# Optimization experiments

Measured on AMD Instinct MI355X. Metric: run time of the kernel, lower is better.

Reference implementation:

```python
import jax, jax.numpy as jnp
import numpy as np

# ---- Cl(4,1) Cayley table (conformal GA: metric +,+,+,+,-) ----
_METRIC = (1.0, 1.0, 1.0, 1.0, -1.0)

def _reorder_sign(a, b):
    # sign from counting swaps to bring blade product to canonical order
    a >>= 1
    s = 0
    while a:
        s += bin(a & b).count("1")
        a >>= 1
    return -1.0 if (s & 1) else 1.0

def _build_cayley():
    C = np.zeros((32, 32, 32), dtype=np.float32)
    for a in range(32):
        for b in range(32):
            s = _reorder_sign(a, b)
            common = a & b
            for i in range(5):
                if (common >> i) & 1:
                    s *= _METRIC[i]
            C[a, b, a ^ b] += s
    return C

CAYLEY = _build_cayley()  # [32,32,32]; out_k = sum_ij C[i,j,k] x_i y_j

EPS = 1e-8

def normalize_cl41(x):
    n = jnp.sqrt(jnp.sum(x * x, axis=-1, keepdims=True))
    return x / (n + EPS)


def setup_inputs() -> dict:
    key = jax.random.key(0)
    k_x, k_wi, k_bi, k_wo, k_bo = jax.random.split(key, 5)
    B, S, D, H = 64, 2048, 6, 8
    x = jax.random.normal(k_x, (B, S, D), dtype=jnp.float32)
    W_in = jax.random.normal(k_wi, (D, H * 32), dtype=jnp.float32) * (1.0 / np.sqrt(D))
    b_in = jax.random.normal(k_bi, (H * 32,), dtype=jnp.float32) * 0.01
    W_out = jax.random.normal(k_wo, (H * 32, 32), dtype=jnp.float32) * (1.0 / np.sqrt(H * 32))
    b_out = jax.random.normal(k_bo, (32,), dtype=jnp.float32) * 0.01
    return {"x": x, "W_in": W_in, "b_in": b_in, "W_out": W_out, "b_out": b_out}


def reference(x, W_in, b_in, W_out, b_out):
    B, S, D = x.shape
    H = W_in.shape[1] // 32
    C = jnp.asarray(CAYLEY)
    # project inputs to per-channel multivectors: (B,S,H,32)
    u = (x @ W_in + b_in).reshape(B, S, H, 32)
    # initial rotor state: identity (scalar blade = 1)
    psi0 = jnp.zeros((B, H, 32), dtype=x.dtype).at[..., 0].set(1.0)

    def step(psi, u_t):  # u_t: (B,H,32)
        delta = normalize_cl41(u_t.at[..., 0].add(1.0))
        psi = normalize_cl41(jnp.einsum("bhi,bhj,ijk->bhk", delta, psi, C))
        return psi, psi

    _, psi_seq = jax.lax.scan(step, psi0, jnp.swapaxes(u, 0, 1))  # (S,B,H,32)
    out = normalize_cl41(psi_seq.reshape(S, B, H * 32) @ W_out + b_out)  # (S,B,32)
    return jnp.swapaxes(out, 0, 1)  # (B,S,32)
```

## Files before the change

### kernel.cpp

```cpp
#include <hip/hip_runtime.h>
#include <hip/hip_bf16.h>
#include <stdint.h>

#define BB 64
#define SS 2048
#define DD 6
#define HH 8
#define NCH 512
#define CHUNKS 256
#define LCH 8

typedef unsigned short ushort_t;
typedef __attribute__((ext_vector_type(8))) __bf16 bf16x8;
typedef __attribute__((ext_vector_type(4))) float f32x4;

struct SignTab { float s[32][32]; };

constexpr int popc5_c(unsigned v) {
    int c = 0;
    for (int i = 0; i < 5; ++i) c += (v >> i) & 1u;
    return c;
}

constexpr SignTab make_signs() {
    SignTab t{};
    for (int a = 0; a < 32; ++a) {
        for (int b = 0; b < 32; ++b) {
            int cnt = 0;
            unsigned aa = ((unsigned)a) >> 1;
            while (aa) { cnt += popc5_c(aa & (unsigned)b); aa >>= 1; }
            if ((a & b) & 16) cnt += 1;
            t.s[a][b] = (cnt & 1) ? -1.0f : 1.0f;
        }
    }
    return t;
}

constexpr SignTab SGN = make_signs();

__device__ __forceinline__ void gp_cl41(const float* __restrict__ a,
                                        const float* __restrict__ b,
                                        float* __restrict__ o) {
#pragma unroll
    for (int k = 0; k < 32; ++k) o[k] = 0.0f;
#pragma unroll
    for (int i = 0; i < 32; ++i) {
#pragma unroll
        for (int k = 0; k < 32; ++k) {
            o[k] = fmaf(SGN.s[i][i ^ k] * a[i], b[i ^ k], o[k]);
        }
    }
}

__device__ __forceinline__ float sumsq32(const float* v) {
    float n0 = 0.f, n1 = 0.f, n2 = 0.f, n3 = 0.f;
#pragma unroll
    for (int k = 0; k < 32; k += 4) {
        n0 = fmaf(v[k+0], v[k+0], n0);
        n1 = fmaf(v[k+1], v[k+1], n1);
        n2 = fmaf(v[k+2], v[k+2], n2);
        n3 = fmaf(v[k+3], v[k+3], n3);
    }
    return (n0 + n1) + (n2 + n3);
}

__device__ __forceinline__ float rsq(float n) {
    return __builtin_amdgcn_rsqf(n);
}

__device__ __forceinline__ uint32_t f2bf_rne(float f) {
    uint32_t u = __float_as_uint(f);
    return (u + 0x7FFFu + ((u >> 16) & 1u)) >> 16;
}

__device__ __forceinline__ uint32_t packh2(float a, float b) {
    union { _Float16 h[2]; uint32_t u; } t;
    t.h[0] = (_Float16)a; t.h[1] = (_Float16)b;
    return t.u;
}
__device__ __forceinline__ float h2lo(uint32_t u) {
    union { uint32_t u32; _Float16 h[2]; } t; t.u32 = u; return (float)t.h[0];
}
__device__ __forceinline__ float h2hi(uint32_t u) {
    union { uint32_t u32; _Float16 h[2]; } t; t.u32 = u; return (float)t.h[1];
}

__device__ __forceinline__ void pack_store16(ushort_t* dst, const float* v, float scale) {
    uint32_t pk[16];
#pragma unroll
    for (int m = 0; m < 16; ++m)
        pk[m] = packh2(v[2*m] * scale, v[2*m+1] * scale);
    uint4* d4 = (uint4*)dst;
#pragma unroll
    for (int m = 0; m < 4; ++m)
        d4[m] = make_uint4(pk[4*m], pk[4*m+1], pk[4*m+2], pk[4*m+3]);
}

__device__ __forceinline__ void load_unpack16(const ushort_t* src, float* v) {
    const uint4* s4 = (const uint4*)src;
#pragma unroll
    for (int m = 0; m < 4; ++m) {
        uint4 t4 = s4[m];
        uint32_t uu[4] = { t4.x, t4.y, t4.z, t4.w };
#pragma unroll
        for (int z = 0; z < 4; ++z) {
            v[8*m + 2*z]     = h2lo(uu[z]);
            v[8*m + 2*z + 1] = h2hi(uu[z]);
        }
    }
}

__global__ __launch_bounds__(256) void k_local(
        const float* __restrict__ x, const float* __restrict__ W_in,
        const float* __restrict__ b_in, ushort_t* __restrict__ psi_loc,
        float* __restrict__ Tbuf) {
    __shared__ float4 sW4[8][57];
    for (int idx = threadIdx.x; idx < 8 * 56; idx += 256) {
        int h = idx / 56, r = idx % 56;
        float4 v;
        if (r < 48) {
            int d = r / 8, j4 = r % 8;
            const float* p = W_in + d * 256 + h * 32 + 4 * j4;
            v = make_float4(p[0], p[1], p[2], p[3]);
        } else {
            const float* p = b_in + h * 32 + 4 * (r - 48);
            v = make_float4(p[0], p[1], p[2], p[3]);
        }
        sW4[h][r] = v;
    }
    __syncthreads();

    int tid = blockIdx.x * 256 + threadIdx.x;
    int c  = tid >> 9;
    int bh = tid & 511;
    int b = bh >> 3, h = bh & 7;

    float4 bias4[8];
#pragma unroll
    for (int j4 = 0; j4 < 8; ++j4) bias4[j4] = sW4[h][48 + j4];

    float p[32];
#pragma unroll
    for (int k = 0; k < 32; ++k) p[k] = 0.f;
    p[0] = 1.f;

    const float* xrow = x + ((size_t)b * SS + (size_t)c * LCH) * DD;
    ushort_t* psi_base = psi_loc + (((size_t)b * SS + (size_t)c * LCH) * HH + h) * 32;

    float xc[12];
    {
        const float4* xp = (const float4*)xrow;
#pragma unroll
        for (int m = 0; m < 3; ++m) {
            float4 t4 = xp[m];
            xc[4*m+0] = t4.x; xc[4*m+1] = t4.y; xc[4*m+2] = t4.z; xc[4*m+3] = t4.w;
        }
    }

#pragma unroll 1
    for (int pr = 0; pr < LCH / 2; ++pr) {
        float x0[6], x1[6];
#pragma unroll
        for (int d = 0; d < 6; ++d) { x0[d] = xc[d]; x1[d] = xc[6 + d]; }

        if (pr < LCH / 2 - 1) {
            const float4* xp = (const float4*)(xrow + (pr + 1) * 12);
#pragma unroll
            for (int m = 0; m < 3; ++m) {
                float4 t4 = xp[m];
                xc[4*m+0] = t4.x; xc[4*m+1] = t4.y; xc[4*m+2] = t4.z; xc[4*m+3] = t4.w;
            }
        }

        float dl0[32], dl1[32];
#pragma unroll
        for (int j4 = 0; j4 < 8; ++j4) {
            float4 bv = bias4[j4];
            dl0[4*j4+0] = bv.x; dl0[4*j4+1] = bv.y; dl0[4*j4+2] = bv.z; dl0[4*j4+3] = bv.w;
            dl1[4*j4+0] = bv.x; dl1[4*j4+1] = bv.y; dl1[4*j4+2] = bv.z; dl1[4*j4+3] = bv.w;
        }
#pragma unroll
        for (int d = 0; d < 6; ++d) {
            float a0 = x0[d], a1 = x1[d];
#pragma unroll
            for (int j4 = 0; j4 < 8; ++j4) {
                float4 w = sW4[h][d * 8 + j4];
                dl0[4*j4+0] = fmaf(a0, w.x, dl0[4*j4+0]);
                dl0[4*j4+1] = fmaf(a0, w.y, dl0[4*j4+1]);
                dl0[4*j4+2] = fmaf(a0, w.z, dl0[4*j4+2]);
                dl0[4*j4+3] = fmaf(a0, w.w, dl0[4*j4+3]);
                dl1[4*j4+0] = fmaf(a1, w.x, dl1[4*j4+0]);
                dl1[4*j4+1] = fmaf(a1, w.y, dl1[4*j4+1]);
                dl1[4*j4+2] = fmaf(a1, w.z, dl1[4*j4+2]);
                dl1[4*j4+3] = fmaf(a1, w.w, dl1[4*j4+3]);
            }
        }
        dl0[0] += 1.0f;
        dl1[0] += 1.0f;

        float o[32];
        gp_cl41(dl0, p, o);
        pack_store16(psi_base + (size_t)(2 * pr) * HH * 32, o, rsq(sumsq32(o)));
        gp_cl41(dl1, o, p);
        pack_store16(psi_base + (size_t)(2 * pr + 1) * HH * 32, p, rsq(sumsq32(p)));
    }

    float inv = rsq(sumsq32(p));
    float* dst = Tbuf + ((size_t)bh * CHUNKS + c) * 32;
#pragma unroll
    for (int k = 0; k < 32; ++k) dst[k] = p[k] * inv;
}

__global__ __launch_bounds__(128) void k_scan_totals(
        const float* __restrict__ Tbuf, float* __restrict__ Ebuf) {
    __shared__ float sT[128][33];
    int chain = blockIdx.x;
    int pp = threadIdx.x;

    float t0[32], t1[32];
    {
        const float* s0 = Tbuf + ((size_t)chain * CHUNKS + 2 * pp) * 32;
#pragma unroll
        for (int k = 0; k < 32; ++k) t0[k] = s0[k];
#pragma unroll
        for (int k = 0; k < 32; ++k) t1[k] = s0[32 + k];
    }

    float v[32];
    {
        float o[32];
        gp_cl41(t1, t0, o);
        float inv = rsq(sumsq32(o));
#pragma unroll
        for (int k = 0; k < 32; ++k) { v[k] = o[k] * inv; sT[pp][k] = v[k]; }
    }
    __syncthreads();

#pragma unroll 1
    for (int off = 1; off < 128; off <<= 1) {
        float w[32];
        bool act = (pp >= off);
        if (act) {
#pragma unroll
            for (int k = 0; k < 32; ++k) w[k] = sT[pp - off][k];
        }
        __syncthreads();
        if (act) {
            float o[32];
            gp_cl41(v, w, o);
            float inv = rsq(sumsq32(o));
#pragma unroll
            for (int k = 0; k < 32; ++k) { v[k] = o[k] * inv; sT[pp][k] = v[k]; }
        }
        __syncthreads();
    }

    float e0[32];
    if (pp == 0) {
#pragma unroll
        for (int k = 0; k < 32; ++k) e0[k] = (k == 0) ? 1.f : 0.f;
    } else {
#pragma unroll
        for (int k = 0; k < 32; ++k) e0[k] = sT[pp - 1][k];
    }
    float e1[32];
    gp_cl41(t0, e0, e1);
    float inv1 = rsq(sumsq32(e1));

    float* d0 = Ebuf + ((size_t)chain * CHUNKS + 2 * pp) * 32;
#pragma unroll
    for (int k = 0; k < 32; ++k) d0[k] = e0[k];
#pragma unroll
    for (int k = 0; k < 32; ++k) d0[32 + k] = e1[k] * inv1;
}

__global__ __launch_bounds__(256) void k_fixup_proj(
        const ushort_t* __restrict__ psi_loc, const float* __restrict__ Ebuf,
        const float* __restrict__ W_out, const float* __restrict__ b_out,
        float* __restrict__ out) {
    int lane = threadIdx.x & 63;
    int wv = threadIdx.x >> 6;
    int q = lane >> 4;
    int n0 = lane & 15;

    bf16x8 Bf[2][8];
#pragma unroll
    for (int nt = 0; nt < 2; ++nt)
#pragma unroll
        for (int kk = 0; kk < 8; ++kk) {
            union { ushort_t u[8]; bf16x8 v; } tmp;
#pragma unroll
            for (int j = 0; j < 8; ++j)
                tmp.u[j] = (ushort_t)f2bf_rne(W_out[(kk * 32 + q * 8 + j) * 32 + nt * 16 + n0]);
            Bf[nt][kk] = tmp.v;
        }
    float bn0 = b_out[n0], bn1 = b_out[16 + n0];

    __shared__ ushort_t psiT[4][16][264];

    int tile = blockIdx.x * 4 + wv;
    int rr0 = tile * 16;
    int b = rr0 >> 11;
    int s0 = rr0 & 2047;

#pragma unroll
    for (int pp = 0; pp < 2; ++pp) {
        int row_local = pp * 8 + (lane >> 3);
        int h = lane & 7;
        int s = s0 + row_local;
        int c = s >> 3;
        int bh = b * 8 + h;

        float a[32], w[32], o[32];
        load_unpack16(psi_loc + (((size_t)b * SS + s) * HH + h) * 32, a);
        const float* e = Ebuf + ((size_t)bh * CHUNKS + c) * 32;
#pragma unroll
        for (int k = 0; k < 32; ++k) w[k] = e[k];

        gp_cl41(a, w, o);
        float inv = rsq(sumsq32(o));

        uint32_t pk[16];
#pragma unroll
        for (int m = 0; m < 16; ++m)
            pk[m] = f2bf_rne(o[2*m] * inv) | (f2bf_rne(o[2*m+1] * inv) << 16);
        uint4* dst = (uint4*)&psiT[wv][row_local][h * 32];
#pragma unroll
        for (int m = 0; m < 4; ++m)
            dst[m] = make_uint4(pk[4*m], pk[4*m+1], pk[4*m+2], pk[4*m+3]);
    }

    __syncthreads();

    f32x4 acc0 = {0.f, 0.f, 0.f, 0.f};
    f32x4 acc1 = {0.f, 0.f, 0.f, 0.f};
#pragma unroll
    for (int kk = 0; kk < 8; ++kk) {
        bf16x8 af = *(const bf16x8*)&psiT[wv][n0][kk * 32 + q * 8];
        acc0 = __builtin_amdgcn_mfma_f32_16x16x32_bf16(af, Bf[0][kk], acc0, 0, 0, 0);
        acc1 = __builtin_amdgcn_mfma_f32_16x16x32_bf16(af, Bf[1][kk], acc1, 0, 0, 0);
    }

    float c0[4], c1[4], ss[4];
#pragma unroll
    for (int i = 0; i < 4; ++i) {
        c0[i] = acc0[i] + bn0;
        c1[i] = acc1[i] + bn1;
        ss[i] = c0[i] * c0[i] + c1[i] * c1[i];
    }
#pragma unroll
    for (int m = 1; m < 16; m <<= 1) {
#pragma unroll
        for (int i = 0; i < 4; ++i) ss[i] += __shfl_xor(ss[i], m);
    }
#pragma unroll
    for (int i = 0; i < 4; ++i) {
        float inv = rsq(ss[i]);
        int row = rr0 + q * 4 + i;
        out[(size_t)row * 32 + n0]      = c0[i] * inv;
        out[(size_t)row * 32 + 16 + n0] = c1[i] * inv;
    }
}

extern "C" void kernel_launch(void* const* d_in, const int* in_sizes, int n_in,
                              void* d_out, int out_size, void* d_ws, size_t ws_size,
                              hipStream_t stream) {
    const float* x     = (const float*)d_in[0];
    const float* W_in  = (const float*)d_in[1];
    const float* b_in  = (const float*)d_in[2];
    const float* W_out = (const float*)d_in[3];
    const float* b_out = (const float*)d_in[4];
    float* out = (float*)d_out;

    char* ws = (char*)d_ws;
    ushort_t* psi  = (ushort_t*)ws;
    float* Tbuf = (float*)(ws + (size_t)64 * 1024 * 1024);
    float* Ebuf = Tbuf;

    k_local      <<< 512, 256, 0, stream>>>(x, W_in, b_in, psi, Tbuf);
    k_scan_totals<<< 512, 128, 0, stream>>>(Tbuf, Ebuf);
    k_fixup_proj <<<2048, 256, 0, stream>>>(psi, Ebuf, W_out, b_out, out);
}
```

Baseline: 203.7 us.

## Recompute local rotor scan in projection kernel instead of storing per-step psi

Result: slower. 423.8 us (+108.1%).

```diff
diff --git a/kernel.cpp b/kernel.cpp
--- a/kernel.cpp
+++ b/kernel.cpp
@@ -7,8 +7,8 @@
 #define DD 6
 #define HH 8
 #define NCH 512
-#define CHUNKS 256
-#define LCH 8
+#define CHUNKS 512
+#define LCH 4
 
 typedef unsigned short ushort_t;
 typedef __attribute__((ext_vector_type(8))) __bf16 bf16x8;
@@ -73,48 +73,38 @@
     return (u + 0x7FFFu + ((u >> 16) & 1u)) >> 16;
 }
 
-__device__ __forceinline__ uint32_t packh2(float a, float b) {
-    union { _Float16 h[2]; uint32_t u; } t;
-    t.h[0] = (_Float16)a; t.h[1] = (_Float16)b;
-    return t.u;
-}
-__device__ __forceinline__ float h2lo(uint32_t u) {
-    union { uint32_t u32; _Float16 h[2]; } t; t.u32 = u; return (float)t.h[0];
-}
-__device__ __forceinline__ float h2hi(uint32_t u) {
-    union { uint32_t u32; _Float16 h[2]; } t; t.u32 = u; return (float)t.h[1];
-}
-
-__device__ __forceinline__ void pack_store16(ushort_t* dst, const float* v, float scale) {
-    uint32_t pk[16];
-#pragma unroll
-    for (int m = 0; m < 16; ++m)
-        pk[m] = packh2(v[2*m] * scale, v[2*m+1] * scale);
-    uint4* d4 = (uint4*)dst;
-#pragma unroll
-    for (int m = 0; m < 4; ++m)
-        d4[m] = make_uint4(pk[4*m], pk[4*m+1], pk[4*m+2], pk[4*m+3]);
-}
-
-__device__ __forceinline__ void load_unpack16(const ushort_t* src, float* v) {
-    const uint4* s4 = (const uint4*)src;
-#pragma unroll
-    for (int m = 0; m < 4; ++m) {
-        uint4 t4 = s4[m];
-        uint32_t uu[4] = { t4.x, t4.y, t4.z, t4.w };
-#pragma unroll
-        for (int z = 0; z < 4; ++z) {
-            v[8*m + 2*z]     = h2lo(uu[z]);
-            v[8*m + 2*z + 1] = h2hi(uu[z]);
-        }
-    }
-}
-
-__global__ __launch_bounds__(256) void k_local(
-        const float* __restrict__ x, const float* __restrict__ W_in,
-        const float* __restrict__ b_in, ushort_t* __restrict__ psi_loc,
-        float* __restrict__ Tbuf) {
-    __shared__ float4 sW4[8][57];
+__device__ __forceinline__ void delta_pair(const float4 (*sW4)[57], int h,
+                                           const float* x0, const float* x1,
+                                           float* dl0, float* dl1) {
+#pragma unroll
+    for (int j4 = 0; j4 < 8; ++j4) {
+        float4 bv = sW4[h][48 + j4];
+        dl0[4*j4+0] = bv.x; dl0[4*j4+1] = bv.y; dl0[4*j4+2] = bv.z; dl0[4*j4+3] = bv.w;
+        dl1[4*j4+0] = bv.x; dl1[4*j4+1] = bv.y; dl1[4*j4+2] = bv.z; dl1[4*j4+3] = bv.w;
+    }
+#pragma unroll
+    for (int d = 0; d < 6; ++d) {
+        float a0 = x0[d], a1 = x1[d];
+#pragma unroll
+        for (int j4 = 0; j4 < 8; ++j4) {
+            float4 w = sW4[h][d * 8 + j4];
+            dl0[4*j4+0] = fmaf(a0, w.x, dl0[4*j4+0]);
+            dl0[4*j4+1] = fmaf(a0, w.y, dl0[4*j4+1]);
+            dl0[4*j4+2] = fmaf(a0, w.z, dl0[4*j4+2]);
+            dl0[4*j4+3] = fmaf(a0, w.w, dl0[4*j4+3]);
+            dl1[4*j4+0] = fmaf(a1, w.x, dl1[4*j4+0]);
+            dl1[4*j4+1] = fmaf(a1, w.y, dl1[4*j4+1]);
+            dl1[4*j4+2] = fmaf(a1, w.z, dl1[4*j4+2]);
+            dl1[4*j4+3] = fmaf(a1, w.w, dl1[4*j4+3]);
+        }
+    }
+    dl0[0] += 1.0f;
+    dl1[0] += 1.0f;
+}
+
+__device__ __forceinline__ void stage_W(const float* __restrict__ W_in,
+                                        const float* __restrict__ b_in,
+                                        float4 (*sW4)[57]) {
     for (int idx = threadIdx.x; idx < 8 * 56; idx += 256) {
         int h = idx / 56, r = idx % 56;
         float4 v;
@@ -128,6 +118,13 @@
         }
         sW4[h][r] = v;
     }
+}
+
+__global__ __launch_bounds__(256, 3) void k_totals(
+        const float* __restrict__ x, const float* __restrict__ W_in,
+        const float* __restrict__ b_in, float* __restrict__ Tbuf) {
+    __shared__ float4 sW4[8][57];
+    stage_W(W_in, b_in, sW4);
     __syncthreads();
 
     int tid = blockIdx.x * 256 + threadIdx.x;
@@ -135,74 +132,28 @@
     int bh = tid & 511;
     int b = bh >> 3, h = bh & 7;
 
-    float4 bias4[8];
-#pragma unroll
-    for (int j4 = 0; j4 < 8; ++j4) bias4[j4] = sW4[h][48 + j4];
-
     float p[32];
 #pragma unroll
     for (int k = 0; k < 32; ++k) p[k] = 0.f;
     p[0] = 1.f;
 
     const float* xrow = x + ((size_t)b * SS + (size_t)c * LCH) * DD;
-    ushort_t* psi_base = psi_loc + (((size_t)b * SS + (size_t)c * LCH) * HH + h) * 32;
-
-    float xc[12];
-    {
-        const float4* xp = (const float4*)xrow;
+
+#pragma unroll
+    for (int pr = 0; pr < 2; ++pr) {
+        float xc[12];
+        const float4* xp = (const float4*)(xrow + pr * 12);
 #pragma unroll
         for (int m = 0; m < 3; ++m) {
             float4 t4 = xp[m];
             xc[4*m+0] = t4.x; xc[4*m+1] = t4.y; xc[4*m+2] = t4.z; xc[4*m+3] = t4.w;
         }
-    }
-
-#pragma unroll 1
-    for (int pr = 0; pr < LCH / 2; ++pr) {
-        float x0[6], x1[6];
-#pragma unroll
-        for (int d = 0; d < 6; ++d) { x0[d] = xc[d]; x1[d] = xc[6 + d]; }
-
-        if (pr < LCH / 2 - 1) {
-            const float4* xp = (const float4*)(xrow + (pr + 1) * 12);
-#pragma unroll
-            for (int m = 0; m < 3; ++m) {
-                float4 t4 = xp[m];
-                xc[4*m+0] = t4.x; xc[4*m+1] = t4.y; xc[4*m+2] = t4.z; xc[4*m+3] = t4.w;
-            }
-        }
-
         float dl0[32], dl1[32];
-#pragma unroll
-        for (int j4 = 0; j4 < 8; ++j4) {
-            float4 bv = bias4[j4];
-            dl0[4*j4+0] = bv.x; dl0[4*j4+1] = bv.y; dl0[4*j4+2] = bv.z; dl0[4*j4+3] = bv.w;
-            dl1[4*j4+0] = bv.x; dl1[4*j4+1] = bv.y; dl1[4*j4+2] = bv.z; dl1[4*j4+3] = bv.w;
-        }
-#pragma unroll
-        for (int d = 0; d < 6; ++d) {
-            float a0 = x0[d], a1 = x1[d];
-#pragma unroll
-            for (int j4 = 0; j4 < 8; ++j4) {
-                float4 w = sW4[h][d * 8 + j4];
-                dl0[4*j4+0] = fmaf(a0, w.x, dl0[4*j4+0]);
-                dl0[4*j4+1] = fmaf(a0, w.y, dl0[4*j4+1]);
-                dl0[4*j4+2] = fmaf(a0, w.z, dl0[4*j4+2]);
-                dl0[4*j4+3] = fmaf(a0, w.w, dl0[4*j4+3]);
-                dl1[4*j4+0] = fmaf(a1, w.x, dl1[4*j4+0]);
-                dl1[4*j4+1] = fmaf(a1, w.y, dl1[4*j4+1]);
-                dl1[4*j4+2] = fmaf(a1, w.z, dl1[4*j4+2]);
-                dl1[4*j4+3] = fmaf(a1, w.w, dl1[4*j4+3]);
-            }
-        }
-        dl0[0] += 1.0f;
-        dl1[0] += 1.0f;
+        delta_pair(sW4, h, xc, xc + 6, dl0, dl1);
 
         float o[32];
         gp_cl41(dl0, p, o);
-        pack_store16(psi_base + (size_t)(2 * pr) * HH * 32, o, rsq(sumsq32(o)));
         gp_cl41(dl1, o, p);
-        pack_store16(psi_base + (size_t)(2 * pr + 1) * HH * 32, p, rsq(sumsq32(p)));
     }
 
     float inv = rsq(sumsq32(p));
@@ -211,9 +162,9 @@
     for (int k = 0; k < 32; ++k) dst[k] = p[k] * inv;
 }
 
-__global__ __launch_bounds__(128) void k_scan_totals(
+__global__ __launch_bounds__(256) void k_scan_totals(
         const float* __restrict__ Tbuf, float* __restrict__ Ebuf) {
-    __shared__ float sT[128][33];
+    __shared__ float sT[256][33];
     int chain = blockIdx.x;
     int pp = threadIdx.x;
 
@@ -237,7 +188,7 @@
     __syncthreads();
 
 #pragma unroll 1
-    for (int off = 1; off < 128; off <<= 1) {
+    for (int off = 1; off < 256; off <<= 1) {
         float w[32];
         bool act = (pp >= off);
         if (act) {
@@ -274,15 +225,94 @@
     for (int k = 0; k < 32; ++k) d0[32 + k] = e1[k] * inv1;
 }
 
-__global__ __launch_bounds__(256) void k_fixup_proj(
-        const ushort_t* __restrict__ psi_loc, const float* __restrict__ Ebuf,
+__global__ __launch_bounds__(256) void k_fused(
+        const float* __restrict__ x, const float* __restrict__ W_in,
+        const float* __restrict__ b_in, const float* __restrict__ Ebuf,
         const float* __restrict__ W_out, const float* __restrict__ b_out,
         float* __restrict__ out) {
-    int lane = threadIdx.x & 63;
-    int wv = threadIdx.x >> 6;
+    __shared__ ushort_t psiT[128][264];
+    __shared__ float4 sW4[8][57];
+    __shared__ float sX[768];
+    float* carrF = (float*)&psiT[0][0];
+
+    int rr0 = blockIdx.x * 128;
+    int b = rr0 >> 11;
+    int s0 = rr0 & 2047;
+    int c0 = s0 >> 2;
+
+    stage_W(W_in, b_in, sW4);
+    {
+        const float4* xg = (const float4*)(x + ((size_t)b * SS + s0) * DD);
+        for (int idx = threadIdx.x; idx < 192; idx += 256)
+            ((float4*)sX)[idx] = xg[idx];
+    }
+#pragma unroll
+    for (int m = 0; m < 32; ++m) {
+        int idx = threadIdx.x + m * 256;
+        int hs = idx >> 10;
+        int off = idx & 1023;
+        carrF[hs * 1032 + off] =
+            Ebuf[(((size_t)(b * 8 + hs)) * CHUNKS + c0) * 32 + off];
+    }
+    __syncthreads();
+
+    int t = threadIdx.x;
+    int h = t & 7, cl = t >> 3;
+
+    float p[32];
+    {
+        const float* cf = carrF + h * 1032 + cl * 32;
+#pragma unroll
+        for (int k = 0; k < 32; ++k) p[k] = cf[k];
+    }
+    __syncthreads();
+
+#pragma unroll
+    for (int pr = 0; pr < 2; ++pr) {
+        int r0 = cl * 4 + 2 * pr;
+        float xc[12];
+        {
+            const float* xs = sX + r0 * 6;
+#pragma unroll
+            for (int d = 0; d < 6; ++d) {
+                float2 t2 = *(const float2*)(xs + 2 * d);
+                xc[2*d] = t2.x; xc[2*d+1] = t2.y;
+            }
+        }
+        float dl0[32], dl1[32];
+        delta_pair(sW4, h, xc, xc + 6, dl0, dl1);
+
+        float o[32];
+        gp_cl41(dl0, p, o);
+        {
+            float inv = rsq(sumsq32(o));
+            uint32_t pk[16];
+#pragma unroll
+            for (int m = 0; m < 16; ++m)
+                pk[m] = f2bf_rne(o[2*m] * inv) | (f2bf_rne(o[2*m+1] * inv) << 16);
+            uint4* dst = (uint4*)&psiT[r0][h * 32];
+#pragma unroll
+            for (int m = 0; m < 4; ++m)
+                dst[m] = make_uint4(pk[4*m], pk[4*m+1], pk[4*m+2], pk[4*m+3]);
+        }
+        gp_cl41(dl1, o, p);
+        {
+            float inv = rsq(sumsq32(p));
+            uint32_t pk[16];
+#pragma unroll
+            for (int m = 0; m < 16; ++m)
+                pk[m] = f2bf_rne(p[2*m] * inv) | (f2bf_rne(p[2*m+1] * inv) << 16);
+            uint4* dst = (uint4*)&psiT[r0 + 1][h * 32];
+#pragma unroll
+            for (int m = 0; m < 4; ++m)
+                dst[m] = make_uint4(pk[4*m], pk[4*m+1], pk[4*m+2], pk[4*m+3]);
+        }
+    }
+
+    int lane = t & 63;
+    int wv = t >> 6;
     int q = lane >> 4;
     int n0 = lane & 15;
-
     bf16x8 Bf[2][8];
 #pragma unroll
     for (int nt = 0; nt < 2; ++nt)
@@ -296,69 +326,41 @@
         }
     float bn0 = b_out[n0], bn1 = b_out[16 + n0];
 
-    __shared__ ushort_t psiT[4][16][264];
-
-    int tile = blockIdx.x * 4 + wv;
-    int rr0 = tile * 16;
-    int b = rr0 >> 11;
-    int s0 = rr0 & 2047;
-
-#pragma unroll
-    for (int pp = 0; pp < 2; ++pp) {
-        int row_local = pp * 8 + (lane >> 3);
-        int h = lane & 7;
-        int s = s0 + row_local;
-        int c = s >> 3;
-        int bh = b * 8 + h;
-
-        float a[32], w[32], o[32];
-        load_unpack16(psi_loc + (((size_t)b * SS + s) * HH + h) * 32, a);
-        const float* e = Ebuf + ((size_t)bh * CHUNKS + c) * 32;
-#pragma unroll
-        for (int k = 0; k < 32; ++k) w[k] = e[k];
-
-        gp_cl41(a, w, o);
-        float inv = rsq(sumsq32(o));
-
-        uint32_t pk[16];
-#pragma unroll
-        for (int m = 0; m < 16; ++m)
-            pk[m] = f2bf_rne(o[2*m] * inv) | (f2bf_rne(o[2*m+1] * inv) << 16);
-        uint4* dst = (uint4*)&psiT[wv][row_local][h * 32];
-#pragma unroll
-        for (int m = 0; m < 4; ++m)
-            dst[m] = make_uint4(pk[4*m], pk[4*m+1], pk[4*m+2], pk[4*m+3]);
-    }
-
-    __syncthreads();
-
-    f32x4 acc0 = {0.f, 0.f, 0.f, 0.f};
-    f32x4 acc1 = {0.f, 0.f, 0.f, 0.f};
-#pragma unroll
-    for (int kk = 0; kk < 8; ++kk) {
-        bf16x8 af = *(const bf16x8*)&psiT[wv][n0][kk * 32 + q * 8];
-        acc0 = __builtin_amdgcn_mfma_f32_16x16x32_bf16(af, Bf[0][kk], acc0, 0, 0, 0);
-        acc1 = __builtin_amdgcn_mfma_f32_16x16x32_bf16(af, Bf[1][kk], acc1, 0, 0, 0);
-    }
-
-    float c0[4], c1[4], ss[4];
-#pragma unroll
-    for (int i = 0; i < 4; ++i) {
-        c0[i] = acc0[i] + bn0;
-        c1[i] = acc1[i] + bn1;
-        ss[i] = c0[i] * c0[i] + c1[i] * c1[i];
-    }
-#pragma unroll
-    for (int m = 1; m < 16; m <<= 1) {
-#pragma unroll
-        for (int i = 0; i < 4; ++i) ss[i] += __shfl_xor(ss[i], m);
-    }
-#pragma unroll
-    for (int i = 0; i < 4; ++i) {
-        float inv = rsq(ss[i]);
-        int row = rr0 + q * 4 + i;
-        out[(size_t)row * 32 + n0]      = c0[i] * inv;
-        out[(size_t)row * 32 + 16 + n0] = c1[i] * inv;
+    __syncthreads();
+
+#pragma unroll
+    for (int tt = 0; tt < 2; ++tt) {
+        int tl = wv * 2 + tt;
+        int r16 = tl * 16;
+
+        f32x4 acc0 = {0.f, 0.f, 0.f, 0.f};
+        f32x4 acc1 = {0.f, 0.f, 0.f, 0.f};
+#pragma unroll
+        for (int kk = 0; kk < 8; ++kk) {
+            bf16x8 af = *(const bf16x8*)&psiT[r16 + n0][kk * 32 + q * 8];
+            acc0 = __builtin_amdgcn_mfma_f32_16x16x32_bf16(af, Bf[0][kk], acc0, 0, 0, 0);
+            acc1 = __builtin_amdgcn_mfma_f32_16x16x32_bf16(af, Bf[1][kk], acc1, 0, 0, 0);
+        }
+
+        float c0v[4], c1v[4], ss[4];
+#pragma unroll
+        for (int i = 0; i < 4; ++i) {
+            c0v[i] = acc0[i] + bn0;
+            c1v[i] = acc1[i] + bn1;
+            ss[i] = c0v[i] * c0v[i] + c1v[i] * c1v[i];
+        }
+#pragma unroll
+        for (int m = 1; m < 16; m <<= 1) {
+#pragma unroll
+            for (int i = 0; i < 4; ++i) ss[i] += __shfl_xor(ss[i], m);
+        }
+#pragma unroll
+        for (int i = 0; i < 4; ++i) {
+            float inv = rsq(ss[i]);
+            int row = rr0 + r16 + q * 4 + i;
+            out[(size_t)row * 32 + n0]      = c0v[i] * inv;
+            out[(size_t)row * 32 + 16 + n0] = c1v[i] * inv;
+        }
     }
 }
 
@@ -372,12 +374,10 @@
     const float* b_out = (const float*)d_in[4];
     float* out = (float*)d_out;
 
-    char* ws = (char*)d_ws;
-    ushort_t* psi  = (ushort_t*)ws;
-    float* Tbuf = (float*)(ws + (size_t)64 * 1024 * 1024);
+    float* Tbuf = (float*)d_ws;
     float* Ebuf = Tbuf;
 
-    k_local      <<< 512, 256, 0, stream>>>(x, W_in, b_in, psi, Tbuf);
-    k_scan_totals<<< 512, 128, 0, stream>>>(Tbuf, Ebuf);
-    k_fixup_proj <<<2048, 256, 0, stream>>>(psi, Ebuf, W_out, b_out, out);
-}
+    k_totals     <<<1024, 256, 0, stream>>>(x, W_in, b_in, Tbuf);
+    k_scan_totals<<< 512, 256, 0, stream>>>(Tbuf, Ebuf);
+    k_fused      <<<1024, 256, 0, stream>>>(x, W_in, b_in, Ebuf, W_out, b_out, out);
+}
```
